# Kernel tuning notes

Measured on AMD Instinct MI355X. Metric: run time of the kernel, lower is better.

The kernel has to match this reference:

```python
import jax, jax.numpy as jnp
import numpy as np

H = 2048        # hidden_size
E = 32          # n_routed_experts
I = 1024        # moe_intermediate_size
TOPK = 6        # num_experts_per_tok
NGROUP = 8      # n_group
TOPKG = 4       # topk_group
SHARED_I = 1024 # moe_intermediate_size * n_shared_experts
SCALE = 2.5     # routed_scaling_factor
T = 1024        # num_tokens


def setup_inputs() -> dict:
    key = jax.random.key(0)
    ks = jax.random.split(key, 7)
    s = 0.02
    return {
        "hidden_states": jax.random.normal(ks[0], (T, H), jnp.float32),
        "gate_w": jax.random.normal(ks[1], (H, E), jnp.float32) * s,
        "e_bias": jax.random.normal(ks[2], (E,), jnp.float32) * s,
        "w_gate_up": jax.random.normal(ks[3], (E, H, 2 * I), jnp.float32) * s,
        "w_down": jax.random.normal(ks[4], (E, I, H), jnp.float32) * s,
        "shared_gate_up": jax.random.normal(ks[5], (H, 2 * SHARED_I), jnp.float32) * s,
        "shared_down": jax.random.normal(ks[6], (SHARED_I, H), jnp.float32) * s,
    }


def _silu_and_mul(gu):
    g, u = jnp.split(gu, 2, axis=-1)
    return jax.nn.silu(g) * u


def _grouped_topk(logits, bias):
    # DeepSeek-V3 style 'noaux_tc' grouped top-k with sigmoid scoring.
    Tn, En = logits.shape
    scores = jax.nn.sigmoid(logits)                 # [T, E]
    scores_choice = scores + bias                   # biased scores used for selection only
    gsize = En // NGROUP
    grp = scores_choice.reshape(Tn, NGROUP, gsize)
    # group score = sum of top-2 biased scores within each group
    group_scores = jnp.sum(jax.lax.top_k(grp, 2)[0], axis=-1)   # [T, G]
    _, gidx = jax.lax.top_k(group_scores, TOPKG)                # [T, topk_group]
    gmask = jnp.sum(jax.nn.one_hot(gidx, NGROUP, dtype=scores.dtype), axis=1)  # [T, G]
    emask = jnp.repeat(gmask, gsize, axis=1)                    # [T, E]
    masked = jnp.where(emask > 0, scores_choice, -jnp.inf)
    _, topk_ids = jax.lax.top_k(masked, TOPK)                   # [T, top_k]
    # weights come from the UNbiased scores, then renormalized (norm_topk_prob=True)
    topk_w = jnp.take_along_axis(scores, topk_ids, axis=1)
    topk_w = topk_w / jnp.sum(topk_w, axis=-1, keepdims=True)
    return topk_w, topk_ids


def _moe_forward(hidden_states, gate_w, e_bias, w_gate_up, w_down,
                 shared_gate_up, shared_down):
    Tn, _ = hidden_states.shape
    # shared expert MLP (reduce_results=False path, fp32 -> no 1/scale correction)
    shared = _silu_and_mul(hidden_states @ shared_gate_up) @ shared_down
    # router
    logits = hidden_states @ gate_w
    topk_w, topk_ids = _grouped_topk(logits, e_bias)
    # sparse combine weights [T, E] (zero except top-k entries)
    combine = jnp.zeros((Tn, E), dtype=hidden_states.dtype)
    combine = combine.at[jnp.arange(Tn)[:, None], topk_ids].add(topk_w)
    # scan over experts, accumulating weighted expert-MLP outputs
    def body(acc, p):
        wgu, wd, w_e = p  # [H,2I], [I,H], [T]
        y = _silu_and_mul(hidden_states @ wgu) @ wd
        return acc + w_e[:, None] * y, None
    out, _ = jax.lax.scan(body, jnp.zeros_like(hidden_states),
                          (w_gate_up, w_down, combine.T))
    return out * SCALE + shared


def reference(hidden_states, gate_w, e_bias, w_gate_up, w_down,
              shared_gate_up, shared_down):
    return _moe_forward(hidden_states, gate_w, e_bias, w_gate_up, w_down,
                        shared_gate_up, shared_down)
```

## Files before the change

kernel.cpp:

```cpp
#include <hip/hip_runtime.h>
#include <stdint.h>

#define TT 1024
#define HH 2048
#define NE 32
#define II 1024
#define NTOPK 6
#define SCALEF 2.5f

typedef __attribute__((ext_vector_type(4))) float f32x4;
typedef __attribute__((ext_vector_type(8))) __bf16 bf16x8;
typedef unsigned short us;

#define GLD16(g, l)                                                                         \
  __builtin_amdgcn_global_load_lds((const __attribute__((address_space(1))) void*)(g),      \
                                   (__attribute__((address_space(3))) void*)(l), 16, 0, 0)

__device__ __forceinline__ unsigned bf16rne(float f) {
    unsigned u = __builtin_bit_cast(unsigned, f);
    return (u + 0x7FFFu + ((u >> 16) & 1u)) >> 16;
}
__device__ __forceinline__ unsigned pack2(float lo, float hi) {
    return bf16rne(lo) | (bf16rne(hi) << 16);
}

__global__ void init_convert(const float* __restrict__ x, us* __restrict__ xb,
                             int* __restrict__ cnt, int* __restrict__ tlist,
                             float* __restrict__ twgt) {
    int gid = blockIdx.x * 256 + threadIdx.x;
    const float4* x4 = (const float4*)x;
    float4 v = x4[gid];
    uint2 o;
    o.x = pack2(v.x, v.y);
    o.y = pack2(v.z, v.w);
    ((uint2*)xb)[gid] = o;
    if (gid < TT) {
        tlist[(NE << 10) + gid] = gid;
        twgt[(NE << 10) + gid] = 1.0f;
    }
    if (gid == 0) cnt[NE] = TT;
}

__global__ void router_kernel(const float* __restrict__ x, const float* __restrict__ gw,
                              const float* __restrict__ bias, int* __restrict__ cnt,
                              int* __restrict__ tlist, float* __restrict__ twgt) {
    int t = blockIdx.x;
    int lane = threadIdx.x;
    int e = lane & 31, h = lane >> 5;
    const float* xr = x + (size_t)t * HH;
    float acc = 0.f;
    #pragma unroll 4
    for (int k = h; k < HH; k += 2)
        acc += xr[k] * gw[k * NE + e];
    acc += __shfl_down(acc, 32);

    __shared__ float sc[NE], sb[NE];
    if (lane < NE) {
        float s = 1.f / (1.f + expf(-acc));
        sc[e] = s;
        sb[e] = s + bias[e];
    }
    __syncthreads();
    if (lane == 0) {
        float gs[8];
        for (int g = 0; g < 8; g++) {
            float m1 = -1e30f, m2 = -1e30f;
            for (int j = 0; j < 4; j++) {
                float v = sb[g * 4 + j];
                if (v > m1) { m2 = m1; m1 = v; }
                else if (v > m2) { m2 = v; }
            }
            gs[g] = m1 + m2;
        }
        unsigned gmask = 0;
        for (int r = 0; r < 4; r++) {
            float best = -1e30f; int bi = 0;
            for (int g = 0; g < 8; g++)
                if (!((gmask >> g) & 1) && gs[g] > best) { best = gs[g]; bi = g; }
            gmask |= 1u << bi;
        }
        int ids[NTOPK]; float wsv[NTOPK]; float sum = 0.f;
        unsigned sel = 0;
        for (int r = 0; r < NTOPK; r++) {
            float best = -1e30f; int bi = 0;
            for (int ee = 0; ee < NE; ee++) {
                if (!((gmask >> (ee >> 2)) & 1)) continue;
                if ((sel >> ee) & 1) continue;
                if (sb[ee] > best) { best = sb[ee]; bi = ee; }
            }
            sel |= 1u << bi;
            ids[r] = bi; wsv[r] = sc[bi]; sum += sc[bi];
        }
        float inv = SCALEF / sum;
        for (int r = 0; r < NTOPK; r++) {
            int ee = ids[r];
            int slot = atomicAdd(&cnt[ee], 1);
            tlist[(ee << 10) + slot] = t;
            twgt[(ee << 10) + slot] = wsv[r] * inv;
        }
    }
}

__global__ __launch_bounds__(256, 3)
void gu_gemm(const us* __restrict__ xb,
             const float* __restrict__ wgu, const float* __restrict__ shgu,
             const int* __restrict__ tlist, const float* __restrict__ twgt,
             const int* __restrict__ cnt, us* __restrict__ act) {
    int e = blockIdx.z;
    int count = cnt[e];
    int m0 = blockIdx.y * 128;
    if (m0 >= count) return;
    int n0 = blockIdx.x * 64;
    const float* wb = (e < NE) ? (wgu + (size_t)e * HH * (2 * II)) : shgu;
    const int* tl = tlist + (e << 10);

    __shared__ __align__(16) us xs[2][128 * 32];
    __shared__ __align__(16) us wg[2][64 * 40];
    __shared__ __align__(16) us wu[2][64 * 40];

    int tid = threadIdx.x;
    int lane = tid & 63, wv = tid >> 6;
    int q = lane >> 4, c = lane & 15;

    int arow = wv * 16 + (lane >> 2);
    int akc = (lane & 3) * 8;
    int tok0 = (m0 + arow < count) ? tl[m0 + arow] : 0;
    int tok1 = (m0 + arow + 64 < count) ? tl[m0 + arow + 64] : 0;
    const us* ag0 = xb + (size_t)tok0 * HH + akc;
    const us* ag1 = xb + (size_t)tok1 * HH + akc;
    int aoff0 = (wv * 16) * 32;
    int aoff1 = (64 + wv * 16) * 32;

    int kp = tid & 15, ig = tid >> 4;
    int n4 = ig * 4;
    const float* wpbase = wb + (size_t)(kp * 2) * (2 * II) + n0 + n4;
    int di = n4 * 20 + kp;

    f32x4 accg[2][4] = {};
    f32x4 accu[2][4] = {};

    GLD16(ag0, xs[0] + aoff0);
    GLD16(ag1, xs[0] + aoff1);
    float4 g0 = *(const float4*)(wpbase);
    float4 g1 = *(const float4*)(wpbase + 2 * II);
    float4 u0 = *(const float4*)(wpbase + II);
    float4 u1 = *(const float4*)(wpbase + 2 * II + II);

    int cur = 0;
    for (int k0 = 0; k0 < HH; k0 += 32) {
        unsigned* wgd = (unsigned*)wg[cur];
        unsigned* wud = (unsigned*)wu[cur];
        wgd[di]      = pack2(g0.x, g1.x);
        wgd[di + 20] = pack2(g0.y, g1.y);
        wgd[di + 40] = pack2(g0.z, g1.z);
        wgd[di + 60] = pack2(g0.w, g1.w);
        wud[di]      = pack2(u0.x, u1.x);
        wud[di + 20] = pack2(u0.y, u1.y);
        wud[di + 40] = pack2(u0.z, u1.z);
        wud[di + 60] = pack2(u0.w, u1.w);
        __syncthreads();

        int k1 = k0 + 32;
        if (k1 < HH) {
            GLD16(ag0 + k1, xs[cur ^ 1] + aoff0);
            GLD16(ag1 + k1, xs[cur ^ 1] + aoff1);
            const float* wp = wpbase + (size_t)k1 * (2 * II);
            g0 = *(const float4*)(wp);
            g1 = *(const float4*)(wp + 2 * II);
            u0 = *(const float4*)(wp + II);
            u1 = *(const float4*)(wp + 2 * II + II);
        }

        const us* xsc = xs[cur];
        const us* wgc = wg[cur];
        const us* wuc = wu[cur];
        bf16x8 a0 = *(const bf16x8*)(xsc + (wv * 32 + c) * 32 + q * 8);
        bf16x8 a1 = *(const bf16x8*)(xsc + (wv * 32 + 16 + c) * 32 + q * 8);
        #pragma unroll
        for (int tn = 0; tn < 4; tn++) {
            bf16x8 bg = *(const bf16x8*)(wgc + (tn * 16 + c) * 40 + q * 8);
            bf16x8 bu = *(const bf16x8*)(wuc + (tn * 16 + c) * 40 + q * 8);
            accg[0][tn] = __builtin_amdgcn_mfma_f32_16x16x32_bf16(a0, bg, accg[0][tn], 0, 0, 0);
            accg[1][tn] = __builtin_amdgcn_mfma_f32_16x16x32_bf16(a1, bg, accg[1][tn], 0, 0, 0);
            accu[0][tn] = __builtin_amdgcn_mfma_f32_16x16x32_bf16(a0, bu, accu[0][tn], 0, 0, 0);
            accu[1][tn] = __builtin_amdgcn_mfma_f32_16x16x32_bf16(a1, bu, accu[1][tn], 0, 0, 0);
        }
        cur ^= 1;
    }

    const float* twp = twgt + (e << 10);
    #pragma unroll
    for (int tm = 0; tm < 2; tm++) {
        int mlb = wv * 32 + tm * 16 + q * 4;
        #pragma unroll
        for (int r = 0; r < 4; r++) {
            int m = m0 + mlb + r;
            if (m < count) {
                float w = twp[m];
                size_t rowbase = ((size_t)(e << 10) + m) * II + n0;
                #pragma unroll
                for (int tn = 0; tn < 4; tn++) {
                    float g = accg[tm][tn][r];
                    float u = accu[tm][tn][r];
                    float a = (g / (1.f + __expf(-g))) * u * w;
                    act[rowbase + tn * 16 + c] = (us)bf16rne(a);
                }
            }
        }
    }
}

__global__ __launch_bounds__(256, 3)
void down_gemm(const us* __restrict__ act,
               const float* __restrict__ wd, const float* __restrict__ shd,
               const int* __restrict__ tlist, const int* __restrict__ cnt,
               float* __restrict__ out) {
    int e = blockIdx.z;
    int count = cnt[e];
    int m0 = blockIdx.y * 128;
    if (m0 >= count) return;
    int n0 = blockIdx.x * 128;
    const float* wb = (e < NE) ? (wd + (size_t)e * II * HH) : shd;
    const int* tl = tlist + (e << 10);

    __shared__ __align__(16) us as_[2][128 * 32];
    __shared__ __align__(16) us bs[2][128 * 40];

    int tid = threadIdx.x;
    int lane = tid & 63, wv = tid >> 6;
    int q = lane >> 4, c = lane & 15;

    const us* ag =
        act + ((size_t)(e << 10) + m0 + wv * 16 + (lane >> 2)) * II + (lane & 3) * 8;
    int aoff0 = (wv * 16) * 32;
    int aoff1 = (64 + wv * 16) * 32;

    int kp = tid & 15, ig = tid >> 4;
    int n4 = ig * 4;
    const float* wpbase = wb + (size_t)(kp * 2) * HH + n0 + n4;
    int di0 = n4 * 20 + kp;
    int di1 = (n4 + 64) * 20 + kp;

    f32x4 acc[2][8] = {};

    GLD16(ag, as_[0] + aoff0);
    GLD16(ag + (size_t)64 * II, as_[0] + aoff1);
    float4 x0 = *(const float4*)(wpbase);
    float4 x1 = *(const float4*)(wpbase + HH);
    float4 y0 = *(const float4*)(wpbase + 64);
    float4 y1 = *(const float4*)(wpbase + HH + 64);

    int cur = 0;
    for (int k0 = 0; k0 < II; k0 += 32) {
        unsigned* bd = (unsigned*)bs[cur];
        bd[di0]      = pack2(x0.x, x1.x);
        bd[di0 + 20] = pack2(x0.y, x1.y);
        bd[di0 + 40] = pack2(x0.z, x1.z);
        bd[di0 + 60] = pack2(x0.w, x1.w);
        bd[di1]      = pack2(y0.x, y1.x);
        bd[di1 + 20] = pack2(y0.y, y1.y);
        bd[di1 + 40] = pack2(y0.z, y1.z);
        bd[di1 + 60] = pack2(y0.w, y1.w);
        __syncthreads();

        int k1 = k0 + 32;
        if (k1 < II) {
            GLD16(ag + k1, as_[cur ^ 1] + aoff0);
            GLD16(ag + (size_t)64 * II + k1, as_[cur ^ 1] + aoff1);
            const float* wp = wpbase + (size_t)k1 * HH;
            x0 = *(const float4*)(wp);
            x1 = *(const float4*)(wp + HH);
            y0 = *(const float4*)(wp + 64);
            y1 = *(const float4*)(wp + HH + 64);
        }

        const us* asc = as_[cur];
        const us* bsc = bs[cur];
        bf16x8 a0 = *(const bf16x8*)(asc + (wv * 32 + c) * 32 + q * 8);
        bf16x8 a1 = *(const bf16x8*)(asc + (wv * 32 + 16 + c) * 32 + q * 8);
        #pragma unroll
        for (int tn = 0; tn < 8; tn++) {
            bf16x8 b = *(const bf16x8*)(bsc + (tn * 16 + c) * 40 + q * 8);
            acc[0][tn] = __builtin_amdgcn_mfma_f32_16x16x32_bf16(a0, b, acc[0][tn], 0, 0, 0);
            acc[1][tn] = __builtin_amdgcn_mfma_f32_16x16x32_bf16(a1, b, acc[1][tn], 0, 0, 0);
        }
        cur ^= 1;
    }

    #pragma unroll
    for (int tm = 0; tm < 2; tm++) {
        int mlb = wv * 32 + tm * 16 + q * 4;
        #pragma unroll
        for (int r = 0; r < 4; r++) {
            int m = m0 + mlb + r;
            if (m < count) {
                int tok = tl[m];
                float* op = out + (size_t)tok * HH + n0 + c;
                #pragma unroll
                for (int tn = 0; tn < 8; tn++)
                    unsafeAtomicAdd(op + tn * 16, acc[tm][tn][r]);
            }
        }
    }
}

extern "C" void kernel_launch(void* const* d_in, const int* in_sizes, int n_in,
                              void* d_out, int out_size, void* d_ws, size_t ws_size,
                              hipStream_t stream) {
    const float* x    = (const float*)d_in[0];
    const float* gw   = (const float*)d_in[1];
    const float* bias = (const float*)d_in[2];
    const float* wgu  = (const float*)d_in[3];
    const float* wd   = (const float*)d_in[4];
    const float* shgu = (const float*)d_in[5];
    const float* shd  = (const float*)d_in[6];
    float* out = (float*)d_out;

    char* ws = (char*)d_ws;
    int*   cnt   = (int*)ws;
    int*   tlist = (int*)(ws + 256);
    float* twgt  = (float*)(ws + 256 + 33 * 1024 * 4);
    us* xb  = (us*)(ws + 256 + 2 * 33 * 1024 * 4);
    us* act = (us*)((char*)xb + (size_t)TT * HH * 2);

    hipMemsetAsync(cnt, 0, 256, stream);
    hipMemsetAsync(out, 0, (size_t)out_size * sizeof(float), stream);
    init_convert<<<dim3((TT * HH / 4) / 256), 256, 0, stream>>>(x, xb, cnt, tlist, twgt);
    router_kernel<<<dim3(TT), 64, 0, stream>>>(x, gw, bias, cnt, tlist, twgt);
    gu_gemm<<<dim3(II / 64, 8, NE + 1), 256, 0, stream>>>(xb, wgu, shgu, tlist, twgt, cnt, act);
    down_gemm<<<dim3(HH / 128, 8, NE + 1), 256, 0, stream>>>(act, wd, shd, tlist, cnt, out);
}
```

Before: 1.230 ms.

## Reshape MoE GEMM tiles to 256 rows to cut redundant weight loads

Changes both expert GEMM kernels from 128-row by 64/128-column tiles to 256-row by 32/64-column tiles, with each wave handling 64 rows. Since most experts receive fewer than 256 tokens, each fp32 weight tile is now streamed and converted to bf16 once per expert instead of twice. This reduces the dominant weight-bandwidth cost. In exchange, more MFMA work is spent on padded rows, and the larger LDS A-tiles may limit occupancy.

```diff
diff --git a/kernel.cpp b/kernel.cpp
--- a/kernel.cpp
+++ b/kernel.cpp
@@ -108,90 +108,91 @@
              const int* __restrict__ cnt, us* __restrict__ act) {
     int e = blockIdx.z;
     int count = cnt[e];
-    int m0 = blockIdx.y * 128;
+    int m0 = blockIdx.y * 256;
     if (m0 >= count) return;
-    int n0 = blockIdx.x * 64;
+    int n0 = blockIdx.x * 32;
     const float* wb = (e < NE) ? (wgu + (size_t)e * HH * (2 * II)) : shgu;
     const int* tl = tlist + (e << 10);
 
-    __shared__ __align__(16) us xs[2][128 * 32];
-    __shared__ __align__(16) us wg[2][64 * 40];
-    __shared__ __align__(16) us wu[2][64 * 40];
+    __shared__ __align__(16) us xs[2][256 * 32];
+    __shared__ __align__(16) us ws_[2][2][32 * 40];
 
     int tid = threadIdx.x;
     int lane = tid & 63, wv = tid >> 6;
     int q = lane >> 4, c = lane & 15;
-
-    int arow = wv * 16 + (lane >> 2);
-    int akc = (lane & 3) * 8;
-    int tok0 = (m0 + arow < count) ? tl[m0 + arow] : 0;
-    int tok1 = (m0 + arow + 64 < count) ? tl[m0 + arow + 64] : 0;
-    const us* ag0 = xb + (size_t)tok0 * HH + akc;
-    const us* ag1 = xb + (size_t)tok1 * HH + akc;
-    int aoff0 = (wv * 16) * 32;
-    int aoff1 = (64 + wv * 16) * 32;
-
-    int kp = tid & 15, ig = tid >> 4;
-    int n4 = ig * 4;
-    const float* wpbase = wb + (size_t)(kp * 2) * (2 * II) + n0 + n4;
-    int di = n4 * 20 + kp;
-
-    f32x4 accg[2][4] = {};
-    f32x4 accu[2][4] = {};
-
-    GLD16(ag0, xs[0] + aoff0);
-    GLD16(ag1, xs[0] + aoff1);
-    float4 g0 = *(const float4*)(wpbase);
-    float4 g1 = *(const float4*)(wpbase + 2 * II);
-    float4 u0 = *(const float4*)(wpbase + II);
-    float4 u1 = *(const float4*)(wpbase + 2 * II + II);
+    int rsub = lane >> 2, j = lane & 3;
+
+    const us* ag[4];
+    int aoff[4];
+    #pragma unroll
+    for (int r = 0; r < 4; r++) {
+        int row = r * 64 + wv * 16 + rsub;
+        int m = m0 + row;
+        int tok = (m < count) ? tl[m] : 0;
+        ag[r] = xb + (size_t)tok * HH + j * 8;
+        aoff[r] = (r * 64 + wv * 16) * 32;
+    }
+
+    int kp = tid & 15;
+    int ig = (tid >> 4) & 7;
+    int half = tid >> 7;
+    const float* wpbase = wb + (size_t)(kp * 2) * (2 * II) + half * II + n0 + ig * 4;
+    int di = (ig * 4) * 20 + kp;
+
+    f32x4 accg[4][2] = {};
+    f32x4 accu[4][2] = {};
+
+    #pragma unroll
+    for (int r = 0; r < 4; r++) GLD16(ag[r], xs[0] + aoff[r]);
+    float4 f0 = *(const float4*)(wpbase);
+    float4 f1 = *(const float4*)(wpbase + 2 * II);
 
     int cur = 0;
     for (int k0 = 0; k0 < HH; k0 += 32) {
-        unsigned* wgd = (unsigned*)wg[cur];
-        unsigned* wud = (unsigned*)wu[cur];
-        wgd[di]      = pack2(g0.x, g1.x);
-        wgd[di + 20] = pack2(g0.y, g1.y);
-        wgd[di + 40] = pack2(g0.z, g1.z);
-        wgd[di + 60] = pack2(g0.w, g1.w);
-        wud[di]      = pack2(u0.x, u1.x);
-        wud[di + 20] = pack2(u0.y, u1.y);
-        wud[di + 40] = pack2(u0.z, u1.z);
-        wud[di + 60] = pack2(u0.w, u1.w);
+        unsigned* wdst = (unsigned*)ws_[cur][half];
+        wdst[di]      = pack2(f0.x, f1.x);
+        wdst[di + 20] = pack2(f0.y, f1.y);
+        wdst[di + 40] = pack2(f0.z, f1.z);
+        wdst[di + 60] = pack2(f0.w, f1.w);
         __syncthreads();
 
         int k1 = k0 + 32;
         if (k1 < HH) {
-            GLD16(ag0 + k1, xs[cur ^ 1] + aoff0);
-            GLD16(ag1 + k1, xs[cur ^ 1] + aoff1);
+            #pragma unroll
+            for (int r = 0; r < 4; r++) GLD16(ag[r] + k1, xs[cur ^ 1] + aoff[r]);
             const float* wp = wpbase + (size_t)k1 * (2 * II);
-            g0 = *(const float4*)(wp);
-            g1 = *(const float4*)(wp + 2 * II);
-            u0 = *(const float4*)(wp + II);
-            u1 = *(const float4*)(wp + 2 * II + II);
+            f0 = *(const float4*)(wp);
+            f1 = *(const float4*)(wp + 2 * II);
         }
 
         const us* xsc = xs[cur];
-        const us* wgc = wg[cur];
-        const us* wuc = wu[cur];
-        bf16x8 a0 = *(const bf16x8*)(xsc + (wv * 32 + c) * 32 + q * 8);
-        bf16x8 a1 = *(const bf16x8*)(xsc + (wv * 32 + 16 + c) * 32 + q * 8);
-        #pragma unroll
-        for (int tn = 0; tn < 4; tn++) {
-            bf16x8 bg = *(const bf16x8*)(wgc + (tn * 16 + c) * 40 + q * 8);
-            bf16x8 bu = *(const bf16x8*)(wuc + (tn * 16 + c) * 40 + q * 8);
-            accg[0][tn] = __builtin_amdgcn_mfma_f32_16x16x32_bf16(a0, bg, accg[0][tn], 0, 0, 0);
-            accg[1][tn] = __builtin_amdgcn_mfma_f32_16x16x32_bf16(a1, bg, accg[1][tn], 0, 0, 0);
-            accu[0][tn] = __builtin_amdgcn_mfma_f32_16x16x32_bf16(a0, bu, accu[0][tn], 0, 0, 0);
-            accu[1][tn] = __builtin_amdgcn_mfma_f32_16x16x32_bf16(a1, bu, accu[1][tn], 0, 0, 0);
+        const us* wgc = ws_[cur][0];
+        const us* wuc = ws_[cur][1];
+        bf16x8 a[4];
+        #pragma unroll
+        for (int tm = 0; tm < 4; tm++)
+            a[tm] = *(const bf16x8*)(xsc + (wv * 64 + tm * 16 + c) * 32 + q * 8);
+        bf16x8 bg[2], bu[2];
+        #pragma unroll
+        for (int tn = 0; tn < 2; tn++) {
+            bg[tn] = *(const bf16x8*)(wgc + (tn * 16 + c) * 40 + q * 8);
+            bu[tn] = *(const bf16x8*)(wuc + (tn * 16 + c) * 40 + q * 8);
+        }
+        #pragma unroll
+        for (int tm = 0; tm < 4; tm++) {
+            #pragma unroll
+            for (int tn = 0; tn < 2; tn++) {
+                accg[tm][tn] = __builtin_amdgcn_mfma_f32_16x16x32_bf16(a[tm], bg[tn], accg[tm][tn], 0, 0, 0);
+                accu[tm][tn] = __builtin_amdgcn_mfma_f32_16x16x32_bf16(a[tm], bu[tn], accu[tm][tn], 0, 0, 0);
+            }
         }
         cur ^= 1;
     }
 
     const float* twp = twgt + (e << 10);
     #pragma unroll
-    for (int tm = 0; tm < 2; tm++) {
-        int mlb = wv * 32 + tm * 16 + q * 4;
+    for (int tm = 0; tm < 4; tm++) {
+        int mlb = wv * 64 + tm * 16 + q * 4;
         #pragma unroll
         for (int r = 0; r < 4; r++) {
             int m = m0 + mlb + r;
@@ -199,11 +200,11 @@
                 float w = twp[m];
                 size_t rowbase = ((size_t)(e << 10) + m) * II + n0;
                 #pragma unroll
-                for (int tn = 0; tn < 4; tn++) {
+                for (int tn = 0; tn < 2; tn++) {
                     float g = accg[tm][tn][r];
                     float u = accu[tm][tn][r];
-                    float a = (g / (1.f + __expf(-g))) * u * w;
-                    act[rowbase + tn * 16 + c] = (us)bf16rne(a);
+                    float aa = (g / (1.f + __expf(-g))) * u * w;
+                    act[rowbase + tn * 16 + c] = (us)bf16rne(aa);
                 }
             }
         }
@@ -217,79 +218,79 @@
                float* __restrict__ out) {
     int e = blockIdx.z;
     int count = cnt[e];
-    int m0 = blockIdx.y * 128;
+    int m0 = blockIdx.y * 256;
     if (m0 >= count) return;
-    int n0 = blockIdx.x * 128;
+    int n0 = blockIdx.x * 64;
     const float* wb = (e < NE) ? (wd + (size_t)e * II * HH) : shd;
     const int* tl = tlist + (e << 10);
 
-    __shared__ __align__(16) us as_[2][128 * 32];
-    __shared__ __align__(16) us bs[2][128 * 40];
+    __shared__ __align__(16) us as_[2][256 * 32];
+    __shared__ __align__(16) us bs[2][64 * 40];
 
     int tid = threadIdx.x;
     int lane = tid & 63, wv = tid >> 6;
     int q = lane >> 4, c = lane & 15;
-
-    const us* ag =
-        act + ((size_t)(e << 10) + m0 + wv * 16 + (lane >> 2)) * II + (lane & 3) * 8;
-    int aoff0 = (wv * 16) * 32;
-    int aoff1 = (64 + wv * 16) * 32;
-
-    int kp = tid & 15, ig = tid >> 4;
-    int n4 = ig * 4;
-    const float* wpbase = wb + (size_t)(kp * 2) * HH + n0 + n4;
-    int di0 = n4 * 20 + kp;
-    int di1 = (n4 + 64) * 20 + kp;
-
-    f32x4 acc[2][8] = {};
-
-    GLD16(ag, as_[0] + aoff0);
-    GLD16(ag + (size_t)64 * II, as_[0] + aoff1);
-    float4 x0 = *(const float4*)(wpbase);
-    float4 x1 = *(const float4*)(wpbase + HH);
-    float4 y0 = *(const float4*)(wpbase + 64);
-    float4 y1 = *(const float4*)(wpbase + HH + 64);
+    int rsub = lane >> 2, j = lane & 3;
+
+    const us* ag[4];
+    int aoff[4];
+    #pragma unroll
+    for (int r = 0; r < 4; r++) {
+        int row = r * 64 + wv * 16 + rsub;
+        ag[r] = act + ((size_t)(e << 10) + m0 + row) * II + j * 8;
+        aoff[r] = (r * 64 + wv * 16) * 32;
+    }
+
+    int kp = tid & 15;
+    int ig = (tid >> 4) & 7;
+    int half = tid >> 7;
+    const float* wpbase = wb + (size_t)(kp * 2) * HH + n0 + half * 32 + ig * 4;
+    int di = (half * 32 + ig * 4) * 20 + kp;
+
+    f32x4 acc[4][4] = {};
+
+    #pragma unroll
+    for (int r = 0; r < 4; r++) GLD16(ag[r], as_[0] + aoff[r]);
+    float4 f0 = *(const float4*)(wpbase);
+    float4 f1 = *(const float4*)(wpbase + HH);
 
     int cur = 0;
     for (int k0 = 0; k0 < II; k0 += 32) {
         unsigned* bd = (unsigned*)bs[cur];
-        bd[di0]      = pack2(x0.x, x1.x);
-        bd[di0 + 20] = pack2(x0.y, x1.y);
-        bd[di0 + 40] = pack2(x0.z, x1.z);
-        bd[di0 + 60] = pack2(x0.w, x1.w);
-        bd[di1]      = pack2(y0.x, y1.x);
-        bd[di1 + 20] = pack2(y0.y, y1.y);
-        bd[di1 + 40] = pack2(y0.z, y1.z);
-        bd[di1 + 60] = pack2(y0.w, y1.w);
+        bd[di]      = pack2(f0.x, f1.x);
+        bd[di + 20] = pack2(f0.y, f1.y);
+        bd[di + 40] = pack2(f0.z, f1.z);
+        bd[di + 60] = pack2(f0.w, f1.w);
         __syncthreads();
 
         int k1 = k0 + 32;
         if (k1 < II) {
-            GLD16(ag + k1, as_[cur ^ 1] + aoff0);
-            GLD16(ag + (size_t)64 * II + k1, as_[cur ^ 1] + aoff1);
+            #pragma unroll
+            for (int r = 0; r < 4; r++) GLD16(ag[r] + k1, as_[cur ^ 1] + aoff[r]);
             const float* wp = wpbase + (size_t)k1 * HH;
-            x0 = *(const float4*)(wp);
-            x1 = *(const float4*)(wp + HH);
-            y0 = *(const float4*)(wp + 64);
-            y1 = *(const float4*)(wp + HH + 64);
+            f0 = *(const float4*)(wp);
+            f1 = *(const float4*)(wp + HH);
         }
 
         const us* asc = as_[cur];
         const us* bsc = bs[cur];
-        bf16x8 a0 = *(const bf16x8*)(asc + (wv * 32 + c) * 32 + q * 8);
-        bf16x8 a1 = *(const bf16x8*)(asc + (wv * 32 + 16 + c) * 32 + q * 8);
-        #pragma unroll
-        for (int tn = 0; tn < 8; tn++) {
+        bf16x8 a[4];
+        #pragma unroll
+        for (int tm = 0; tm < 4; tm++)
+            a[tm] = *(const bf16x8*)(asc + (wv * 64 + tm * 16 + c) * 32 + q * 8);
+        #pragma unroll
+        for (int tn = 0; tn < 4; tn++) {
             bf16x8 b = *(const bf16x8*)(bsc + (tn * 16 + c) * 40 + q * 8);
-            acc[0][tn] = __builtin_amdgcn_mfma_f32_16x16x32_bf16(a0, b, acc[0][tn], 0, 0, 0);
-            acc[1][tn] = __builtin_amdgcn_mfma_f32_16x16x32_bf16(a1, b, acc[1][tn], 0, 0, 0);
+            #pragma unroll
+            for (int tm = 0; tm < 4; tm++)
+                acc[tm][tn] = __builtin_amdgcn_mfma_f32_16x16x32_bf16(a[tm], b, acc[tm][tn], 0, 0, 0);
         }
         cur ^= 1;
     }
 
     #pragma unroll
-    for (int tm = 0; tm < 2; tm++) {
-        int mlb = wv * 32 + tm * 16 + q * 4;
+    for (int tm = 0; tm < 4; tm++) {
+        int mlb = wv * 64 + tm * 16 + q * 4;
         #pragma unroll
         for (int r = 0; r < 4; r++) {
             int m = m0 + mlb + r;
@@ -297,7 +298,7 @@
                 int tok = tl[m];
                 float* op = out + (size_t)tok * HH + n0 + c;
                 #pragma unroll
-                for (int tn = 0; tn < 8; tn++)
+                for (int tn = 0; tn < 4; tn++)
                     unsafeAtomicAdd(op + tn * 16, acc[tm][tn][r]);
             }
         }
@@ -327,6 +328,6 @@
     hipMemsetAsync(out, 0, (size_t)out_size * sizeof(float), stream);
     init_convert<<<dim3((TT * HH / 4) / 256), 256, 0, stream>>>(x, xb, cnt, tlist, twgt);
     router_kernel<<<dim3(TT), 64, 0, stream>>>(x, gw, bias, cnt, tlist, twgt);
-    gu_gemm<<<dim3(II / 64, 8, NE + 1), 256, 0, stream>>>(xb, wgu, shgu, tlist, twgt, cnt, act);
-    down_gemm<<<dim3(HH / 128, 8, NE + 1), 256, 0, stream>>>(act, wd, shd, tlist, cnt, out);
-}
+    gu_gemm<<<dim3(II / 32, 4, NE + 1), 256, 0, stream>>>(xb, wgu, shgu, tlist, twgt, cnt, act);
+    down_gemm<<<dim3(HH / 64, 4, NE + 1), 256, 0, stream>>>(act, wd, shd, tlist, cnt, out);
+}
```

New measurement: 1.269 ms. +3.1%, slower.
